# Kernel optimization log

Measured on AMD Instinct MI355X. Metric: run time of the kernel, lower is better.

The kernel has to match this reference:

```python
import jax, jax.numpy as jnp
import numpy as np
from jax import lax

N_QUBITS = 8
DEPTH = 2
IN_DIM = 512
LN_EPS = 1e-5


def _ry_shared(state, w, theta_w):
    # RY(theta) on wire w, shared angle across the batch. state: [B, 2,...,2]
    ax = w + 1
    c = jnp.cos(theta_w / 2)
    s = jnp.sin(theta_w / 2)
    s0 = lax.index_in_dim(state, 0, axis=ax, keepdims=True)
    s1 = lax.index_in_dim(state, 1, axis=ax, keepdims=True)
    return jnp.concatenate([c * s0 - s * s1, s * s0 + c * s1], axis=ax)


def _cnot(state, cw, tw):
    # CNOT control=cw, target=tw. state: [B, 2,...,2]
    ax_c = cw + 1
    ax_t = tw + 1
    s0 = lax.index_in_dim(state, 0, axis=ax_c, keepdims=True)
    s1 = lax.index_in_dim(state, 1, axis=ax_c, keepdims=True)
    s1 = jnp.flip(s1, axis=ax_t)
    return jnp.concatenate([s0, s1], axis=ax_c)


def _circuit(angles, theta):
    # angles: [B, n]; theta: [n]. Batched statevector sim (RY/CNOT are real).
    B, n = angles.shape
    half = angles * 0.5
    c = jnp.cos(half)
    s = jnp.sin(half)
    # Initial RY layer on |0...0> is a product state: qubit i -> [cos, sin]
    state = jnp.ones((B,), dtype=angles.dtype)
    for i in range(n):
        amp = jnp.stack([c[:, i], s[:, i]], axis=-1)  # [B, 2]
        state = state[..., None] * amp.reshape((B,) + (1,) * i + (2,))
    # state: [B, 2, 2, ..., 2] (n qubit axes)
    for _ in range(DEPTH):
        for i in range(n):
            state = _cnot(state, i, (i + 1) % n)
        for i in range(n):
            state = _ry_shared(state, i, theta[i])
    # <Z_i> = P(bit_i=0) - P(bit_i=1)
    p = state * state
    zs = []
    for i in range(n):
        axes = tuple(a for a in range(1, n + 1) if a != i + 1)
        m = p.sum(axis=axes)  # [B, 2]
        zs.append(m[:, 0] - m[:, 1])
    return jnp.stack(zs, axis=-1)  # [B, n]


def setup_inputs() -> dict:
    key = jax.random.key(0)
    ks = jax.random.split(key, 6)
    B = 131072
    return {
        "E": jax.random.normal(ks[0], (B, IN_DIM), dtype=jnp.float32),
        "ln_gamma": jnp.ones((IN_DIM,), dtype=jnp.float32),
        "ln_beta": jnp.zeros((IN_DIM,), dtype=jnp.float32),
        "W_pre": jax.random.normal(ks[1], (N_QUBITS, IN_DIM), dtype=jnp.float32) * (1.0 / np.sqrt(IN_DIM)),
        "b_pre": jax.random.normal(ks[2], (N_QUBITS,), dtype=jnp.float32) * 0.02,
        "theta": jax.random.normal(ks[3], (N_QUBITS,), dtype=jnp.float32) * 0.1,
        "W_post": jax.random.normal(ks[4], (1, N_QUBITS), dtype=jnp.float32) * (1.0 / np.sqrt(N_QUBITS)),
        "b_post": jax.random.normal(ks[5], (1,), dtype=jnp.float32) * 0.02,
    }


def reference(E, ln_gamma, ln_beta, W_pre, b_pre, theta, W_post, b_post):
    # pre: LayerNorm + Linear(in_dim -> n_qubits)
    mu = E.mean(axis=-1, keepdims=True)
    var = ((E - mu) ** 2).mean(axis=-1, keepdims=True)
    x = (E - mu) * lax.rsqrt(var + LN_EPS) * ln_gamma + ln_beta
    angles = x @ W_pre.T + b_pre  # [B, n_qubits]
    Z = _circuit(angles, theta)  # [B, n_qubits]
    logit_known = (Z @ W_post.T + b_post)[:, 0]  # squeeze(-1)
    return logit_known
```

## Files before the change

kernel.cpp:

```cpp
#include <hip/hip_runtime.h>

#define WS_GT    0
#define WS_G     4096
#define WS_K     4104
#define WS_COEF  4112

constexpr void conj_cnot_ce(unsigned &pat, int &sg, int c, int t) {
  unsigned wc = (pat >> (2 * c)) & 3u;
  unsigned wt = (pat >> (2 * t)) & 3u;
  unsigned k = 4u * wc + wt;
  unsigned nc = (0x5F0AF5A0u >> (2u * k)) & 3u;
  unsigned nt = (0xB1E4B1E4u >> (2u * k)) & 3u;
  if ((0x8040u >> k) & 1u) sg = -sg;
  pat &= ~((3u << (2 * c)) | (3u << (2 * t)));
  pat |= (nc << (2 * c)) | (nt << (2 * t));
}
constexpr void conj_ring_ce(unsigned &pat, int &sg) {
  for (int g = 0; g < 8; ++g) {
    int c = 7 - g, t = (c + 1) & 7;
    conj_cnot_ce(pat, sg, c, t);
  }
}

#define MAX_RAW 672
struct CT {
  int nU, nR;
  unsigned short upat[MAX_RAW];
  int ustart[MAX_RAW + 1];
  short rsign[MAX_RAW];
  unsigned char rwi[MAX_RAW];
  unsigned short rcos[MAX_RAW];
  unsigned short rsin[MAX_RAW];
};

constexpr CT build_ct() {
  CT T{};
  unsigned short rpat[MAX_RAW] = {};
  short rsgn[MAX_RAW] = {};
  unsigned char rwi_[MAX_RAW] = {};
  unsigned short rc_[MAX_RAW] = {}, rs_[MAX_RAW] = {};
  int nraw = 0;
  for (int o = 0; o < 16; ++o) {
    const int i = o >> 1, p = o & 1;
    unsigned pat = (p ? 1u : 2u) << (2 * i);
    int sg0 = 1;
    conj_ring_ce(pat, sg0);
    int w = 0;
    for (int q = 0; q < 8; ++q)
      if ((pat >> (2 * q)) & 3u) ++w;
    for (int b = 0; b < (1 << w); ++b) {
      int sign = sg0;
      unsigned ce = 0, se = 0;
      if (p == 0) ce += 1u << (2 * i);
      else { se += 1u << (2 * i); sign = -sign; }
      unsigned np = 0;
      int j = 0;
      for (int q = 0; q < 8; ++q) {
        unsigned L = (pat >> (2 * q)) & 3u;
        if (!L) continue;
        int bb = (b >> j) & 1;
        ++j;
        if (L == 2u) {
          if (bb) { np |= 1u << (2 * q); se += 1u << (2 * q); sign = -sign; }
          else    { np |= 2u << (2 * q); ce += 1u << (2 * q); }
        } else {
          if (bb) { np |= 2u << (2 * q); se += 1u << (2 * q); }
          else    { np |= 1u << (2 * q); ce += 1u << (2 * q); }
        }
      }
      int sg2 = 1;
      conj_ring_ce(np, sg2);
      sign *= sg2;
      bool hasY = false;
      for (int q = 0; q < 8; ++q)
        if (((np >> (2 * q)) & 3u) == 3u) hasY = true;
      if (hasY) continue;
      rpat[nraw] = (unsigned short)np;
      rsgn[nraw] = (short)sign;
      rwi_[nraw] = (unsigned char)i;
      rc_[nraw] = (unsigned short)ce;
      rs_[nraw] = (unsigned short)se;
      ++nraw;
    }
  }
  int map_[65536];
  for (int x = 0; x < 65536; ++x) map_[x] = -1;
  int uid[MAX_RAW] = {};
  int cnt[MAX_RAW] = {};
  int nU = 0;
  for (int r = 0; r < nraw; ++r) {
    int pp = rpat[r];
    if (map_[pp] < 0) { map_[pp] = nU; T.upat[nU] = (unsigned short)pp; ++nU; }
    uid[r] = map_[pp];
    cnt[uid[r]]++;
  }
  T.ustart[0] = 0;
  for (int u = 0; u < nU; ++u) T.ustart[u + 1] = T.ustart[u] + cnt[u];
  int fill[MAX_RAW] = {};
  for (int u = 0; u < nU; ++u) fill[u] = T.ustart[u];
  for (int r = 0; r < nraw; ++r) {
    int pos = fill[uid[r]]++;
    T.rsign[pos] = rsgn[r];
    T.rwi[pos] = rwi_[r];
    T.rcos[pos] = rc_[r];
    T.rsin[pos] = rs_[r];
  }
  T.nU = nU;
  T.nR = nraw;
  return T;
}

static constexpr CT kT = build_ct();

__global__ void qsco_init_kernel(const float* __restrict__ ln_gamma,
                                 const float* __restrict__ ln_beta,
                                 const float* __restrict__ Wpre,
                                 const float* __restrict__ bpre,
                                 const float* __restrict__ theta,
                                 const float* __restrict__ Wpost,
                                 float* __restrict__ ws) {
  const int tid = threadIdx.x;

  for (int i = tid; i < 4096; i += 256) {
    int k = i >> 3, j = i & 7;
    ws[WS_GT + i] = ln_gamma[k] * Wpre[j * 512 + k];
  }
  {
    const int j = tid >> 5, l = tid & 31;
    float gs = 0.f, ks = 0.f;
    for (int t = 0; t < 16; ++t) {
      int k = l * 16 + t;
      float w = Wpre[j * 512 + k];
      gs = fmaf(ln_gamma[k], w, gs);
      ks = fmaf(ln_beta[k], w, ks);
    }
    for (int m = 1; m <= 16; m <<= 1) {
      gs += __shfl_xor(gs, m, 64);
      ks += __shfl_xor(ks, m, 64);
    }
    if (l == 0) {
      ws[WS_G + j] = gs;
      ws[WS_K + j] = ks + bpre[j];
    }
  }
  float cth[8], sth[8];
#pragma unroll
  for (int q = 0; q < 8; ++q) {
    cth[q] = __cosf(theta[q]);
    sth[q] = __sinf(theta[q]);
  }
  for (int u = tid; u < kT.nU; u += 256) {
    float sum = 0.f;
    for (int r = kT.ustart[u]; r < kT.ustart[u + 1]; ++r) {
      float c = (float)kT.rsign[r] * Wpost[kT.rwi[r]];
      unsigned ce = kT.rcos[r], se = kT.rsin[r];
#pragma unroll
      for (int q = 0; q < 8; ++q) {
        int e1 = (ce >> (2 * q)) & 3;
        int e2 = (se >> (2 * q)) & 3;
        if (e1 >= 1) c *= cth[q];
        if (e1 == 2) c *= cth[q];
        if (e2 >= 1) c *= sth[q];
        if (e2 == 2) c *= sth[q];
      }
      sum += c;
    }
    ws[WS_COEF + u] = sum;
  }
}

#define TS 18

__global__ __launch_bounds__(256, 2) void qsco_main_kernel(
    const float* __restrict__ E,
    const float* __restrict__ ws,
    const float* __restrict__ bpost,
    float* __restrict__ out,
    int nrows) {
  __shared__ float tile[4][2][64 * TS];
  const int lane = threadIdx.x & 63;
  const int w = threadIdx.x >> 6;
  const int waveId = blockIdx.x * 4 + w;
  const int r0 = waveId * 64;
  if (r0 >= nrows) return;
  const int myRow = r0 + lane;
  float* bufA = &tile[w][0][0];
  float* bufB = &tile[w][1][0];
  const float* gT = ws + WS_GT;

  float s0 = 0.f, s1 = 0.f;
  float d[8];
#pragma unroll
  for (int j = 0; j < 8; ++j) d[j] = 0.f;

  float4 va[4], vb[4];

#define LOADC(dst, cbase)                                                  \
  { _Pragma("unroll") for (int ii = 0; ii < 4; ++ii) {                     \
      int f = lane + 64 * ii;                                              \
      int rl = f >> 2, kq = f & 3;                                         \
      int rr = min(r0 + rl, nrows - 1);                                    \
      dst[ii] = *(const float4*)(E + (size_t)rr * 512 + (cbase) + kq * 4); \
  } }
#define STOREC(buf, src)                                                   \
  { _Pragma("unroll") for (int ii = 0; ii < 4; ++ii) {                     \
      int f = lane + 64 * ii;                                              \
      int rl = f >> 2, kq = f & 3;                                         \
      float* p = (buf) + rl * TS + kq * 4;                                 \
      *(float2*)(p) = make_float2(src[ii].x, src[ii].y);                   \
      *(float2*)(p + 2) = make_float2(src[ii].z, src[ii].w);               \
  } }
#define COMPUTEC(buf, cbase)                                               \
  { _Pragma("unroll") for (int kk = 0; kk < 16; kk += 2) {                 \
      float2 e2 = *(const float2*)((buf) + lane * TS + kk);                \
      const float* gk = gT + ((cbase) + kk) * 8;                           \
      s0 += e2.x + e2.y;                                                   \
      s1 = fmaf(e2.x, e2.x, fmaf(e2.y, e2.y, s1));                         \
      _Pragma("unroll") for (int j = 0; j < 8; ++j)                        \
        d[j] = fmaf(e2.y, gk[8 + j], fmaf(e2.x, gk[j], d[j]));             \
  } }

  LOADC(va, 0)
  STOREC(bufA, va)
  LOADC(va, 16)
#pragma unroll 1
  for (int cb = 0; cb < 512; cb += 32) {
    if (cb + 32 < 512) LOADC(vb, cb + 32)
    STOREC(bufB, va)
    COMPUTEC(bufA, cb)
    STOREC(bufA, vb)
    if (cb + 48 < 512) LOADC(va, cb + 48)
    COMPUTEC(bufB, cb + 16)
  }

  const float mu = s0 * (1.0f / 512.0f);
  const float var = s1 * (1.0f / 512.0f) - mu * mu;
  const float rstd = rsqrtf(var + 1e-5f);

  const float* Gp = ws + WS_G;
  const float* Kp = ws + WS_K;
  float cA[8], sA[8];
#pragma unroll
  for (int j = 0; j < 8; ++j) {
    float ang = rstd * (d[j] - mu * Gp[j]) + Kp[j];
    cA[j] = __cosf(ang);
    sA[j] = __sinf(ang);
  }

  const float* cf = ws + WS_COEF;
  float acc0 = bpost[0], acc1 = 0.f, acc2 = 0.f, acc3 = 0.f;
#pragma unroll
  for (int u = 0; u < kT.nU; ++u) {
    const unsigned pat = kT.upat[u];
    float prod = cf[u];
#pragma unroll
    for (int q = 0; q < 8; ++q) {
      const unsigned L = (pat >> (2 * q)) & 3u;
      if (L == 1u) prod *= sA[q];
      else if (L == 2u) prod *= cA[q];
    }
    if ((u & 3) == 0) acc0 += prod;
    else if ((u & 3) == 1) acc1 += prod;
    else if ((u & 3) == 2) acc2 += prod;
    else acc3 += prod;
  }
  const float v = (acc0 + acc1) + (acc2 + acc3);
  if (myRow < nrows) out[myRow] = v;

#undef LOADC
#undef STOREC
#undef COMPUTEC
}

extern "C" void kernel_launch(void* const* d_in, const int* in_sizes, int n_in,
                              void* d_out, int out_size, void* d_ws, size_t ws_size,
                              hipStream_t stream) {
  const float* E        = (const float*)d_in[0];
  const float* ln_gamma = (const float*)d_in[1];
  const float* ln_beta  = (const float*)d_in[2];
  const float* Wpre     = (const float*)d_in[3];
  const float* bpre     = (const float*)d_in[4];
  const float* theta    = (const float*)d_in[5];
  const float* Wpost    = (const float*)d_in[6];
  const float* bpost    = (const float*)d_in[7];
  float* out = (float*)d_out;
  float* ws = (float*)d_ws;

  const int nrows = in_sizes[0] / 512;

  qsco_init_kernel<<<1, 256, 0, stream>>>(ln_gamma, ln_beta, Wpre, bpre, theta,
                                          Wpost, ws);

  const int blocks = (nrows + 255) / 256;
  qsco_main_kernel<<<blocks, 256, 0, stream>>>(E, ws, bpost, out, nrows);
}
```

Baseline: 438.3 us.

## Split each row's reduction across two waves and merge partials through LDS

Each block now handles 128 rows, and two waves share each 64-row group by covering one half of the 512 columns each. The partial dot products and moments are combined in shared memory before a single wave evaluates the circuit polynomial. Loads are reorganised into 32-column chunks with 8 float4 loads in flight per lane, staged through a single padded tile per wave. Launch bounds rise to 4 blocks per CU to increase the number of memory requests in flight. This adds a block-wide barrier, and half of the waves sit idle during the epilogue.

```diff
diff --git a/kernel.cpp b/kernel.cpp
--- a/kernel.cpp
+++ b/kernel.cpp
@@ -120,7 +120,6 @@
                                  const float* __restrict__ Wpost,
                                  float* __restrict__ ws) {
   const int tid = threadIdx.x;
-
   for (int i = tid; i < 4096; i += 256) {
     int k = i >> 3, j = i & 7;
     ws[WS_GT + i] = ln_gamma[k] * Wpre[j * 512 + k];
@@ -169,23 +168,32 @@
   }
 }
 
-#define TS 18
-
-__global__ __launch_bounds__(256, 2) void qsco_main_kernel(
+#define TSD 34
+
+__global__ __launch_bounds__(256, 4) void qsco_main_kernel(
     const float* __restrict__ E,
     const float* __restrict__ ws,
     const float* __restrict__ bpost,
     float* __restrict__ out,
     int nrows) {
-  __shared__ float tile[4][2][64 * TS];
+  __shared__ float tile[4][64 * TSD];
   const int lane = threadIdx.x & 63;
   const int w = threadIdx.x >> 6;
-  const int waveId = blockIdx.x * 4 + w;
-  const int r0 = waveId * 64;
-  if (r0 >= nrows) return;
-  const int myRow = r0 + lane;
-  float* bufA = &tile[w][0][0];
-  float* bufB = &tile[w][1][0];
+  const int rg = w >> 1;
+  const int kh = w & 1;
+  const int r0 = blockIdx.x * 128 + rg * 64;
+  const int kb = kh * 256;
+  float* tl = &tile[w][0];
+
+  const int lrow = lane >> 3, lcol = lane & 7;
+  const float* gbase[8];
+#pragma unroll
+  for (int ii = 0; ii < 8; ++ii) {
+    int rr = min(r0 + lrow + 8 * ii, nrows - 1);
+    gbase[ii] = E + (size_t)rr * 512 + kb + lcol * 4;
+  }
+  float* stbase = tl + TSD * lrow + 4 * lcol;
+  const float* rdbase = tl + TSD * lane;
   const float* gT = ws + WS_GT;
 
   float s0 = 0.f, s1 = 0.f;
@@ -193,83 +201,92 @@
 #pragma unroll
   for (int j = 0; j < 8; ++j) d[j] = 0.f;
 
-  float4 va[4], vb[4];
-
-#define LOADC(dst, cbase)                                                  \
-  { _Pragma("unroll") for (int ii = 0; ii < 4; ++ii) {                     \
-      int f = lane + 64 * ii;                                              \
-      int rl = f >> 2, kq = f & 3;                                         \
-      int rr = min(r0 + rl, nrows - 1);                                    \
-      dst[ii] = *(const float4*)(E + (size_t)rr * 512 + (cbase) + kq * 4); \
-  } }
-#define STOREC(buf, src)                                                   \
-  { _Pragma("unroll") for (int ii = 0; ii < 4; ++ii) {                     \
-      int f = lane + 64 * ii;                                              \
-      int rl = f >> 2, kq = f & 3;                                         \
-      float* p = (buf) + rl * TS + kq * 4;                                 \
+  float4 A[8], B[8];
+
+#define LOAD32(dst, c)                                                     \
+  { _Pragma("unroll") for (int ii = 0; ii < 8; ++ii)                       \
+      dst[ii] = *(const float4*)(gbase[ii] + 32 * (c)); }
+#define STORE32(src)                                                       \
+  { _Pragma("unroll") for (int ii = 0; ii < 8; ++ii) {                     \
+      float* p = stbase + 272 * ii;                                        \
       *(float2*)(p) = make_float2(src[ii].x, src[ii].y);                   \
-      *(float2*)(p + 2) = make_float2(src[ii].z, src[ii].w);               \
-  } }
-#define COMPUTEC(buf, cbase)                                               \
-  { _Pragma("unroll") for (int kk = 0; kk < 16; kk += 2) {                 \
-      float2 e2 = *(const float2*)((buf) + lane * TS + kk);                \
-      const float* gk = gT + ((cbase) + kk) * 8;                           \
+      *(float2*)(p + 2) = make_float2(src[ii].z, src[ii].w); } }
+#define COMPUTE32(c)                                                       \
+  { _Pragma("unroll") for (int kk = 0; kk < 32; kk += 2) {                 \
+      float2 e2 = *(const float2*)(rdbase + kk);                           \
+      const float* gk = gT + (kb + 32 * (c) + kk) * 8;                     \
       s0 += e2.x + e2.y;                                                   \
       s1 = fmaf(e2.x, e2.x, fmaf(e2.y, e2.y, s1));                         \
       _Pragma("unroll") for (int j = 0; j < 8; ++j)                        \
-        d[j] = fmaf(e2.y, gk[8 + j], fmaf(e2.x, gk[j], d[j]));             \
-  } }
-
-  LOADC(va, 0)
-  STOREC(bufA, va)
-  LOADC(va, 16)
-#pragma unroll 1
-  for (int cb = 0; cb < 512; cb += 32) {
-    if (cb + 32 < 512) LOADC(vb, cb + 32)
-    STOREC(bufB, va)
-    COMPUTEC(bufA, cb)
-    STOREC(bufA, vb)
-    if (cb + 48 < 512) LOADC(va, cb + 48)
-    COMPUTEC(bufB, cb + 16)
-  }
-
-  const float mu = s0 * (1.0f / 512.0f);
-  const float var = s1 * (1.0f / 512.0f) - mu * mu;
-  const float rstd = rsqrtf(var + 1e-5f);
-
-  const float* Gp = ws + WS_G;
-  const float* Kp = ws + WS_K;
-  float cA[8], sA[8];
-#pragma unroll
-  for (int j = 0; j < 8; ++j) {
-    float ang = rstd * (d[j] - mu * Gp[j]) + Kp[j];
-    cA[j] = __cosf(ang);
-    sA[j] = __sinf(ang);
-  }
-
-  const float* cf = ws + WS_COEF;
-  float acc0 = bpost[0], acc1 = 0.f, acc2 = 0.f, acc3 = 0.f;
-#pragma unroll
-  for (int u = 0; u < kT.nU; ++u) {
-    const unsigned pat = kT.upat[u];
-    float prod = cf[u];
-#pragma unroll
-    for (int q = 0; q < 8; ++q) {
-      const unsigned L = (pat >> (2 * q)) & 3u;
-      if (L == 1u) prod *= sA[q];
-      else if (L == 2u) prod *= cA[q];
-    }
-    if ((u & 3) == 0) acc0 += prod;
-    else if ((u & 3) == 1) acc1 += prod;
-    else if ((u & 3) == 2) acc2 += prod;
-    else acc3 += prod;
-  }
-  const float v = (acc0 + acc1) + (acc2 + acc3);
-  if (myRow < nrows) out[myRow] = v;
-
-#undef LOADC
-#undef STOREC
-#undef COMPUTEC
+        d[j] = fmaf(e2.y, gk[8 + j], fmaf(e2.x, gk[j], d[j])); } }
+
+  LOAD32(A, 0)
+  LOAD32(B, 1)
+  STORE32(A)
+#pragma unroll
+  for (int c = 0; c < 8; ++c) {
+    if (c + 2 < 8) {
+      if (c & 1) { LOAD32(B, c + 2) } else { LOAD32(A, c + 2) }
+    }
+    COMPUTE32(c)
+    if (c + 1 < 8) {
+      if (c & 1) { STORE32(A) } else { STORE32(B) }
+    }
+  }
+
+  if (kh == 1) {
+#pragma unroll
+    for (int j = 0; j < 8; ++j) tl[lane * 12 + j] = d[j];
+    tl[lane * 12 + 8] = s0;
+    tl[lane * 12 + 9] = s1;
+  }
+  __syncthreads();
+  if (kh == 0) {
+    const float* pp = &tile[w + 1][0];
+#pragma unroll
+    for (int j = 0; j < 8; ++j) d[j] += pp[lane * 12 + j];
+    s0 += pp[lane * 12 + 8];
+    s1 += pp[lane * 12 + 9];
+
+    const float mu = s0 * (1.0f / 512.0f);
+    const float var = s1 * (1.0f / 512.0f) - mu * mu;
+    const float rstd = rsqrtf(var + 1e-5f);
+
+    const float* Gp = ws + WS_G;
+    const float* Kp = ws + WS_K;
+    float cA[8], sA[8];
+#pragma unroll
+    for (int j = 0; j < 8; ++j) {
+      float ang = rstd * (d[j] - mu * Gp[j]) + Kp[j];
+      cA[j] = __cosf(ang);
+      sA[j] = __sinf(ang);
+    }
+
+    const float* cf = ws + WS_COEF;
+    float acc0 = bpost[0], acc1 = 0.f, acc2 = 0.f, acc3 = 0.f;
+#pragma unroll
+    for (int u = 0; u < kT.nU; ++u) {
+      const unsigned pat = kT.upat[u];
+      float prod = cf[u];
+#pragma unroll
+      for (int q = 0; q < 8; ++q) {
+        const unsigned L = (pat >> (2 * q)) & 3u;
+        if (L == 1u) prod *= sA[q];
+        else if (L == 2u) prod *= cA[q];
+      }
+      if ((u & 3) == 0) acc0 += prod;
+      else if ((u & 3) == 1) acc1 += prod;
+      else if ((u & 3) == 2) acc2 += prod;
+      else acc3 += prod;
+    }
+    const float v = (acc0 + acc1) + (acc2 + acc3);
+    const int myRow = r0 + lane;
+    if (myRow < nrows) out[myRow] = v;
+  }
+
+#undef LOAD32
+#undef STORE32
+#undef COMPUTE32
 }
 
 extern "C" void kernel_launch(void* const* d_in, const int* in_sizes, int n_in,
@@ -291,6 +308,6 @@
   qsco_init_kernel<<<1, 256, 0, stream>>>(ln_gamma, ln_beta, Wpre, bpre, theta,
                                           Wpost, ws);
 
-  const int blocks = (nrows + 255) / 256;
+  const int blocks = (nrows + 127) / 128;
   qsco_main_kernel<<<blocks, 256, 0, stream>>>(E, ws, bpost, out, nrows);
 }
```

Result: slower. 523.4 us (+19.4%).
